# Optimization experiments

Hardware: AMD Instinct MI355X
Metric: run time of the kernel (lower is better)

Reference implementation:

```python
import jax, jax.numpy as jnp
import numpy as np

B, N, H_IN, H_HID, N_HEAD = 32, 500, 64, 16, 8
N_VALID = 400  # valid (non-padded) nodes per graph; node 0 is the root
NEG_INF = -1e20


def setup_inputs() -> dict:
    key = jax.random.key(0)
    ks = jax.random.split(key, 10)
    x = jax.random.normal(ks[0], (B, N, H_IN), jnp.float32)
    # sparse-ish binary adjacency with self loops
    A = (jax.random.uniform(ks[1], (B, N, N)) < 0.05).astype(jnp.float32)
    A = jnp.maximum(A, jnp.eye(N, dtype=jnp.float32)[None])
    # mask_nonzero: first N_VALID nodes of every graph are valid
    mask_batch = jnp.repeat(jnp.arange(B, dtype=jnp.int32), N_VALID)
    mask_row = jnp.tile(jnp.arange(N_VALID, dtype=jnp.int32), B)
    s = 0.1
    w1 = jax.random.normal(ks[2], (N_HEAD, H_IN, H_HID), jnp.float32) * s
    a_src1 = jax.random.normal(ks[3], (N_HEAD, H_HID), jnp.float32) * s
    a_dst1 = jax.random.normal(ks[4], (N_HEAD, H_HID), jnp.float32) * s
    w2 = jax.random.normal(ks[5], (1, N_HEAD * H_HID, H_IN), jnp.float32) * s
    a_src2 = jax.random.normal(ks[6], (1, H_IN), jnp.float32) * s
    a_dst2 = jax.random.normal(ks[7], (1, H_IN), jnp.float32) * s
    attn_w = jax.random.normal(ks[8], (2 * H_IN,), jnp.float32) * s
    return {"x": x, "A": A, "mask_batch": mask_batch, "mask_row": mask_row,
            "w1": w1, "a_src1": a_src1, "a_dst1": a_dst1,
            "w2": w2, "a_src2": a_src2, "a_dst2": a_dst2, "attn_w": attn_w}


def gat_layer(h_in, A, w, a_src, a_dst):
    # h_in: [B,N,F_in]; w: [H,F_in,F_out]
    h = jnp.einsum('bnf,hfo->bhno', h_in, w)              # [B,H,N,F_out]
    e_src = jnp.einsum('bhno,ho->bhn', h, a_src)          # [B,H,N]
    e_dst = jnp.einsum('bhno,ho->bhn', h, a_dst)
    e = jax.nn.leaky_relu(e_src[..., :, None] + e_dst[..., None, :], 0.2)  # [B,H,N,N]
    e = jnp.where(A[:, None, :, :] > 0, e, NEG_INF)
    attn = jax.nn.softmax(e, axis=-1)
    return jnp.einsum('bhnm,bhmo->bhno', attn, h)         # [B,H,N,F_out]


def reference(x, A, mask_batch, mask_row, w1, a_src1, a_dst1, w2, a_src2, a_dst2, attn_w):
    b, n, _ = x.shape
    # BatchGAT encoder: layer 1 (multi-head, concat + ELU), layer 2 (1 head -> h_in)
    h1 = gat_layer(x, A, w1, a_src1, a_dst1)                       # [B,H,N,h_hid]
    h1 = jax.nn.elu(h1).transpose(0, 2, 1, 3).reshape(b, n, -1)    # [B,N,H*h_hid]
    xc = gat_layer(h1, A, w2, a_src2, a_dst2)[:, 0]                # [B,N,h_in]
    # zero out padded nodes (so their Post_Attn scores are exactly 0)
    valid = jnp.zeros((b, n), x.dtype).at[mask_batch, mask_row].set(1.0)
    xc = xc * valid[:, :, None]
    # Post_Attn: scatter root features to each valid node position
    root = jnp.zeros_like(xc).at[mask_batch, mask_row, :].set(xc[mask_batch, 0, :])
    x_plus = jnp.concatenate([xc, root], axis=-1)                  # [B,N,2*h_in]
    score = x_plus @ attn_w                                        # [B,N]
    score = jnp.where(score == 0, NEG_INF, score)[:, :, None]      # masked_fill
    attn = jax.nn.softmax(score, axis=1)                           # softmax over nodes
    pooled = jnp.einsum('bnf,bn->bf', xc, attn[:, :, 0])           # [B,h_in]
    return pooled, attn
```

## Files before the change

### kernel.cpp

```cpp
#include <hip/hip_runtime.h>

#define NB 32
#define NN 500
#define HIN 64
#define HHID 16
#define NHEAD 8
#define NVALID 400
#define MAXK 128
#define NEG_INF -1e20f

__global__ __launch_bounds__(256) void k_pre(const float* __restrict__ A,
                                             int* __restrict__ nbr, int* __restrict__ cnt,
                                             const float* __restrict__ x, const float* __restrict__ w1,
                                             const float* __restrict__ as1, const float* __restrict__ ad1,
                                             float* __restrict__ h1p, float* __restrict__ e1s,
                                             float* __restrict__ e1d)
{
    int bid = blockIdx.x;
    if (bid < 4000) {
        int row = bid * 4 + (threadIdx.x >> 6);
        int lane = threadIdx.x & 63;
        const float4* arow4 = (const float4*)(A + (size_t)row * NN);
        int* np = nbr + (size_t)row * MAXK;
        int c = 0;
#pragma unroll
        for (int it = 0; it < 2; ++it) {
            int idx = it * 64 + lane;
            float4 av;
            if (idx < 125) av = arow4[idx];
            else { av.x = av.y = av.z = av.w = 0.f; }
            bool v0 = av.x > 0.f, v1 = av.y > 0.f, v2 = av.z > 0.f, v3 = av.w > 0.f;
            unsigned long long b0 = __ballot(v0), b1 = __ballot(v1);
            unsigned long long b2 = __ballot(v2), b3 = __ballot(v3);
            unsigned long long below = (1ull << lane) - 1ull;
            int p = c + __popcll(b0 & below) + __popcll(b1 & below)
                      + __popcll(b2 & below) + __popcll(b3 & below);
            int col = idx * 4;
            if (v0 && p < MAXK) np[p] = col;     p += (int)v0;
            if (v1 && p < MAXK) np[p] = col + 1; p += (int)v1;
            if (v2 && p < MAXK) np[p] = col + 2; p += (int)v2;
            if (v3 && p < MAXK) np[p] = col + 3; p += (int)v3;
            c += (int)(__popcll(b0) + __popcll(b1) + __popcll(b2) + __popcll(b3));
        }
        if (lane == 0) cnt[row] = c < MAXK ? c : MAXK;
        return;
    }
    int pb = bid - 4000;
    int b = pb >> 5, chunk = pb & 31;
    int t = threadIdx.x, slot = t >> 7, lane = t & 127;
    int h = lane >> 4, o = lane & 15;
    float wreg[64];
#pragma unroll
    for (int f = 0; f < 64; ++f) wreg[f] = w1[h * 1024 + f * 16 + o];
    float as_r = as1[h * 16 + o], ad_r = ad1[h * 16 + o];
    __shared__ __align__(16) float xs[16][64];
    {
        int node = chunk * 16 + (t >> 4);
        float4 v = make_float4(0.f, 0.f, 0.f, 0.f);
        if (node < NN) v = *(const float4*)&x[(size_t)(b * NN + node) * HIN + ((t * 4) & 63)];
        *(float4*)&xs[t >> 4][(t * 4) & 63] = v;
    }
    __syncthreads();
    for (int i = 0; i < 8; ++i) {
        int n = chunk * 16 + i * 2 + slot;
        if (n < NN) {
            const float* xrow = xs[i * 2 + slot];
            float acc = 0.f;
#pragma unroll
            for (int f4 = 0; f4 < 16; ++f4) {
                float4 xv = *(const float4*)&xrow[f4 * 4];
                acc += xv.x * wreg[f4 * 4] + xv.y * wreg[f4 * 4 + 1]
                     + xv.z * wreg[f4 * 4 + 2] + xv.w * wreg[f4 * 4 + 3];
            }
            h1p[(size_t)(b * NN + n) * 128 + lane] = acc;
            float vs = acc * as_r, vd = acc * ad_r;
#pragma unroll
            for (int m = 1; m < 16; m <<= 1) { vs += __shfl_xor(vs, m); vd += __shfl_xor(vd, m); }
            if (o == 0) {
                e1s[(size_t)(b * NN + n) * 8 + h] = vs;
                e1d[(size_t)(b * NN + n) * 8 + h] = vd;
            }
        }
    }
}

__global__ __launch_bounds__(128) void k_agg1p2(const int* __restrict__ nbr, const int* __restrict__ cnt,
                                                const float* __restrict__ h1p, const float* __restrict__ e1s,
                                                const float* __restrict__ e1d, const float* __restrict__ w2,
                                                const float* __restrict__ as2, const float* __restrict__ ad2,
                                                float* __restrict__ h2p, float* __restrict__ e2s,
                                                float* __restrict__ e2d)
{
    int bid = blockIdx.x;
    int xcd = bid & 7, g = bid >> 3;
    int b = (g / NN) * 8 + xcd;
    int n = g % NN;
    int row = b * NN + n;
    int t = threadIdx.x;
    int h = t >> 4, o = t & 15;
    int half = t >> 6, o2 = t & 63;
    __shared__ int nb_s[MAXK];
    __shared__ float p_s[NHEAD][MAXK + 4];
    __shared__ __align__(16) float hc[128];
    __shared__ float part[128];
    int K = cnt[row];
    for (int k = t; k < K; k += 128) nb_s[k] = nbr[(size_t)row * MAXK + k];
    __syncthreads();
    float es = e1s[(size_t)row * 8 + h];
    float r[8];
    float mx = -1e30f;
#pragma unroll
    for (int j = 0; j < 8; ++j) {
        int k = o + j * 16;
        if (k < K) {
            float e = es + e1d[(size_t)(b * NN + nb_s[k]) * 8 + h];
            e = e > 0.f ? e : 0.2f * e;
            r[j] = e;
            mx = fmaxf(mx, e);
        }
    }
#pragma unroll
    for (int m = 1; m < 16; m <<= 1) mx = fmaxf(mx, __shfl_xor(mx, m));
    float sum = 0.f;
#pragma unroll
    for (int j = 0; j < 8; ++j) {
        int k = o + j * 16;
        if (k < K) { float v = __expf(r[j] - mx); r[j] = v; sum += v; }
    }
#pragma unroll
    for (int m = 1; m < 16; m <<= 1) sum += __shfl_xor(sum, m);
    float inv = 1.f / sum;
#pragma unroll
    for (int j = 0; j < 8; ++j) {
        int k = o + j * 16;
        if (k < K) p_s[h][k] = r[j] * inv;
    }
    __syncthreads();
    float acc = 0.f;
    const float* hp = h1p + (size_t)b * NN * 128 + t;
    int k = 0;
    for (; k + 8 <= K; k += 8) {
        float a0 = hp[(size_t)nb_s[k] * 128];
        float a1 = hp[(size_t)nb_s[k + 1] * 128];
        float a2 = hp[(size_t)nb_s[k + 2] * 128];
        float a3 = hp[(size_t)nb_s[k + 3] * 128];
        float a4 = hp[(size_t)nb_s[k + 4] * 128];
        float a5 = hp[(size_t)nb_s[k + 5] * 128];
        float a6 = hp[(size_t)nb_s[k + 6] * 128];
        float a7 = hp[(size_t)nb_s[k + 7] * 128];
        acc += p_s[h][k] * a0;
        acc += p_s[h][k + 1] * a1;
        acc += p_s[h][k + 2] * a2;
        acc += p_s[h][k + 3] * a3;
        acc += p_s[h][k + 4] * a4;
        acc += p_s[h][k + 5] * a5;
        acc += p_s[h][k + 6] * a6;
        acc += p_s[h][k + 7] * a7;
    }
    for (; k < K; ++k) acc += p_s[h][k] * hp[(size_t)nb_s[k] * 128];
    hc[t] = acc > 0.f ? acc : expm1f(acc);
    __syncthreads();
    const float* wbase = w2 + (size_t)(half * 64) * 64 + o2;
    float acc2 = 0.f;
#pragma unroll
    for (int j4 = 0; j4 < 16; ++j4) {
        float4 hv = *(const float4*)&hc[half * 64 + j4 * 4];
        acc2 += hv.x * wbase[(j4 * 4 + 0) * 64] + hv.y * wbase[(j4 * 4 + 1) * 64]
              + hv.z * wbase[(j4 * 4 + 2) * 64] + hv.w * wbase[(j4 * 4 + 3) * 64];
    }
    part[t] = acc2;
    __syncthreads();
    if (half == 0) {
        float val = acc2 + part[64 + o2];
        h2p[(size_t)row * 64 + o2] = val;
        float vs = val * as2[o2], vd = val * ad2[o2];
#pragma unroll
        for (int m = 1; m < 64; m <<= 1) { vs += __shfl_xor(vs, m); vd += __shfl_xor(vd, m); }
        if (o2 == 0) { e2s[row] = vs; e2d[row] = vd; }
    }
}

__global__ __launch_bounds__(64) void k_agg2(const int* __restrict__ nbr, const int* __restrict__ cnt,
                                             const float* __restrict__ h2p, const float* __restrict__ e2s,
                                             const float* __restrict__ e2d, const float* __restrict__ aw,
                                             float* __restrict__ xc, float* __restrict__ sc,
                                             float* __restrict__ root_dot)
{
    int bid = blockIdx.x;
    int xcd = bid & 7, g = bid >> 3;
    int b = (g / NN) * 8 + xcd;
    int n = g % NN;
    int row = b * NN + n;
    int t = threadIdx.x;
    if (n >= NVALID) { xc[(size_t)row * 64 + t] = 0.f; return; }
    __shared__ int nb_s[MAXK];
    __shared__ float p_s[MAXK];
    int K = cnt[row];
    int nb0 = 0, nb1 = 0;
    if (t < K)      { nb0 = nbr[(size_t)row * MAXK + t];      nb_s[t] = nb0; }
    if (t + 64 < K) { nb1 = nbr[(size_t)row * MAXK + t + 64]; nb_s[t + 64] = nb1; }
    __syncthreads();
    float es = e2s[row];
    float r0 = -1e30f, r1 = -1e30f;
    if (t < K) {
        float e = es + e2d[b * NN + nb0];
        r0 = e > 0.f ? e : 0.2f * e;
    }
    if (t + 64 < K) {
        float e = es + e2d[b * NN + nb1];
        r1 = e > 0.f ? e : 0.2f * e;
    }
    float mx = fmaxf(r0, r1);
#pragma unroll
    for (int m = 1; m < 64; m <<= 1) mx = fmaxf(mx, __shfl_xor(mx, m));
    float v0 = (t < K) ? __expf(r0 - mx) : 0.f;
    float v1 = (t + 64 < K) ? __expf(r1 - mx) : 0.f;
    float sum = v0 + v1;
#pragma unroll
    for (int m = 1; m < 64; m <<= 1) sum += __shfl_xor(sum, m);
    float inv = 1.f / sum;
    if (t < K) p_s[t] = v0 * inv;
    if (t + 64 < K) p_s[t + 64] = v1 * inv;
    __syncthreads();
    float acc = 0.f;
    const float* h2b = h2p + (size_t)b * NN * 64 + t;
    int k = 0;
    for (; k + 8 <= K; k += 8) {
        float a0 = h2b[(size_t)nb_s[k] * 64];
        float a1 = h2b[(size_t)nb_s[k + 1] * 64];
        float a2 = h2b[(size_t)nb_s[k + 2] * 64];
        float a3 = h2b[(size_t)nb_s[k + 3] * 64];
        float a4 = h2b[(size_t)nb_s[k + 4] * 64];
        float a5 = h2b[(size_t)nb_s[k + 5] * 64];
        float a6 = h2b[(size_t)nb_s[k + 6] * 64];
        float a7 = h2b[(size_t)nb_s[k + 7] * 64];
        acc += p_s[k] * a0;
        acc += p_s[k + 1] * a1;
        acc += p_s[k + 2] * a2;
        acc += p_s[k + 3] * a3;
        acc += p_s[k + 4] * a4;
        acc += p_s[k + 5] * a5;
        acc += p_s[k + 6] * a6;
        acc += p_s[k + 7] * a7;
    }
    for (; k < K; ++k) acc += p_s[k] * h2b[(size_t)nb_s[k] * 64];
    xc[(size_t)row * 64 + t] = acc;
    float v = acc * aw[t];
#pragma unroll
    for (int m = 1; m < 64; m <<= 1) v += __shfl_xor(v, m);
    if (t == 0) sc[row] = v;
    if (n == 0) {
        float v2 = acc * aw[64 + t];
#pragma unroll
        for (int m = 1; m < 64; m <<= 1) v2 += __shfl_xor(v2, m);
        if (t == 0) root_dot[b] = v2;
    }
}

__global__ __launch_bounds__(1024) void k_pool(const float* __restrict__ xc, const float* __restrict__ sc,
                                               const float* __restrict__ root_dot, float* __restrict__ out)
{
    int b = blockIdx.x;
    int t = threadIdx.x, w = t >> 6, lane = t & 63;
    __shared__ float attn_s[NN];
    __shared__ float red[16];
    __shared__ float part[16][64];
    const float* xb = xc + (size_t)b * NN * 64;
    float rd = root_dot[b];
    float s = NEG_INF;
    if (t < NVALID) {
        s = sc[b * NN + t] + rd;
        if (s == 0.f) s = NEG_INF;
    }
    float mx = s;
#pragma unroll
    for (int m = 1; m < 64; m <<= 1) mx = fmaxf(mx, __shfl_xor(mx, m));
    if (lane == 0) red[w] = mx;
    __syncthreads();
    mx = red[0];
#pragma unroll
    for (int i = 1; i < 16; ++i) mx = fmaxf(mx, red[i]);
    float e = (t < NN) ? __expf(s - mx) : 0.f;
    float sum = e;
#pragma unroll
    for (int m = 1; m < 64; m <<= 1) sum += __shfl_xor(sum, m);
    __syncthreads();
    if (lane == 0) red[w] = sum;
    __syncthreads();
    sum = 0.f;
#pragma unroll
    for (int i = 0; i < 16; ++i) sum += red[i];
    float inv = 1.f / sum;
    if (t < NN) {
        float a = e * inv;
        out[NB * 64 + b * NN + t] = a;
        attn_s[t] = a;
    }
    __syncthreads();
    float acc = 0.f;
    for (int n = w; n < NN; n += 16) acc += attn_s[n] * xb[(size_t)n * 64 + lane];
    part[w][lane] = acc;
    __syncthreads();
    if (t < 64) {
        float v = 0.f;
#pragma unroll
        for (int i = 0; i < 16; ++i) v += part[i][t];
        out[b * 64 + t] = v;
    }
}

extern "C" void kernel_launch(void* const* d_in, const int* in_sizes, int n_in,
                              void* d_out, int out_size, void* d_ws, size_t ws_size,
                              hipStream_t stream) {
    const float* x   = (const float*)d_in[0];
    const float* A   = (const float*)d_in[1];
    const float* w1  = (const float*)d_in[4];
    const float* as1 = (const float*)d_in[5];
    const float* ad1 = (const float*)d_in[6];
    const float* w2  = (const float*)d_in[7];
    const float* as2 = (const float*)d_in[8];
    const float* ad2 = (const float*)d_in[9];
    const float* aw  = (const float*)d_in[10];
    float* out = (float*)d_out;

    char* ws = (char*)d_ws;
    int* nbr = (int*)ws;
    int* cnt = (int*)(ws + (size_t)16000 * 128 * 4);
    float* f = (float*)(ws + (size_t)16000 * 129 * 4);
    float* h1p   = f;  f += (size_t)NB * NN * 128;
    float* e1s   = f;  f += (size_t)NB * NN * NHEAD;
    float* e1d   = f;  f += (size_t)NB * NN * NHEAD;
    float* h2p   = f;  f += (size_t)NB * NN * 64;
    float* e2s   = f;  f += (size_t)NB * NN;
    float* e2d   = f;  f += (size_t)NB * NN;
    float* xc    = f;  f += (size_t)NB * NN * 64;
    float* sc    = f;  f += (size_t)NB * NN;
    float* rootd = f;  f += NB;

    hipLaunchKernelGGL(k_pre,    dim3(5024),    dim3(256), 0, stream, A, nbr, cnt, x, w1, as1, ad1, h1p, e1s, e1d);
    hipLaunchKernelGGL(k_agg1p2, dim3(NB * NN), dim3(128), 0, stream, nbr, cnt, h1p, e1s, e1d, w2, as2, ad2, h2p, e2s, e2d);
    hipLaunchKernelGGL(k_agg2,   dim3(NB * NN), dim3(64),  0, stream, nbr, cnt, h2p, e2s, e2d, aw, xc, sc, rootd);
    hipLaunchKernelGGL(k_pool,   dim3(NB),      dim3(1024), 0, stream, xc, sc, rootd, out);
}
```

Before: 159.8 us.

## Fuse second-layer aggregation into pooling kernel and reorder k_pre block roles

```diff
diff --git a/kernel.cpp b/kernel.cpp
--- a/kernel.cpp
+++ b/kernel.cpp
@@ -17,8 +17,8 @@
                                              float* __restrict__ e1d)
 {
     int bid = blockIdx.x;
-    if (bid < 4000) {
-        int row = bid * 4 + (threadIdx.x >> 6);
+    if (bid >= 1024) {
+        int row = (bid - 1024) * 4 + (threadIdx.x >> 6);
         int lane = threadIdx.x & 63;
         const float4* arow4 = (const float4*)(A + (size_t)row * NN);
         int* np = nbr + (size_t)row * MAXK;
@@ -45,7 +45,7 @@
         if (lane == 0) cnt[row] = c < MAXK ? c : MAXK;
         return;
     }
-    int pb = bid - 4000;
+    int pb = bid;
     int b = pb >> 5, chunk = pb & 31;
     int t = threadIdx.x, slot = t >> 7, lane = t & 127;
     int h = lane >> 4, o = lane & 15;
@@ -180,96 +180,88 @@
     }
 }
 
-__global__ __launch_bounds__(64) void k_agg2(const int* __restrict__ nbr, const int* __restrict__ cnt,
-                                             const float* __restrict__ h2p, const float* __restrict__ e2s,
-                                             const float* __restrict__ e2d, const float* __restrict__ aw,
-                                             float* __restrict__ xc, float* __restrict__ sc,
-                                             float* __restrict__ root_dot)
-{
-    int bid = blockIdx.x;
-    int xcd = bid & 7, g = bid >> 3;
-    int b = (g / NN) * 8 + xcd;
-    int n = g % NN;
-    int row = b * NN + n;
-    int t = threadIdx.x;
-    if (n >= NVALID) { xc[(size_t)row * 64 + t] = 0.f; return; }
-    __shared__ int nb_s[MAXK];
-    __shared__ float p_s[MAXK];
-    int K = cnt[row];
-    int nb0 = 0, nb1 = 0;
-    if (t < K)      { nb0 = nbr[(size_t)row * MAXK + t];      nb_s[t] = nb0; }
-    if (t + 64 < K) { nb1 = nbr[(size_t)row * MAXK + t + 64]; nb_s[t + 64] = nb1; }
-    __syncthreads();
-    float es = e2s[row];
-    float r0 = -1e30f, r1 = -1e30f;
-    if (t < K) {
-        float e = es + e2d[b * NN + nb0];
-        r0 = e > 0.f ? e : 0.2f * e;
-    }
-    if (t + 64 < K) {
-        float e = es + e2d[b * NN + nb1];
-        r1 = e > 0.f ? e : 0.2f * e;
-    }
-    float mx = fmaxf(r0, r1);
-#pragma unroll
-    for (int m = 1; m < 64; m <<= 1) mx = fmaxf(mx, __shfl_xor(mx, m));
-    float v0 = (t < K) ? __expf(r0 - mx) : 0.f;
-    float v1 = (t + 64 < K) ? __expf(r1 - mx) : 0.f;
-    float sum = v0 + v1;
-#pragma unroll
-    for (int m = 1; m < 64; m <<= 1) sum += __shfl_xor(sum, m);
-    float inv = 1.f / sum;
-    if (t < K) p_s[t] = v0 * inv;
-    if (t + 64 < K) p_s[t + 64] = v1 * inv;
-    __syncthreads();
-    float acc = 0.f;
-    const float* h2b = h2p + (size_t)b * NN * 64 + t;
-    int k = 0;
-    for (; k + 8 <= K; k += 8) {
-        float a0 = h2b[(size_t)nb_s[k] * 64];
-        float a1 = h2b[(size_t)nb_s[k + 1] * 64];
-        float a2 = h2b[(size_t)nb_s[k + 2] * 64];
-        float a3 = h2b[(size_t)nb_s[k + 3] * 64];
-        float a4 = h2b[(size_t)nb_s[k + 4] * 64];
-        float a5 = h2b[(size_t)nb_s[k + 5] * 64];
-        float a6 = h2b[(size_t)nb_s[k + 6] * 64];
-        float a7 = h2b[(size_t)nb_s[k + 7] * 64];
-        acc += p_s[k] * a0;
-        acc += p_s[k + 1] * a1;
-        acc += p_s[k + 2] * a2;
-        acc += p_s[k + 3] * a3;
-        acc += p_s[k + 4] * a4;
-        acc += p_s[k + 5] * a5;
-        acc += p_s[k + 6] * a6;
-        acc += p_s[k + 7] * a7;
-    }
-    for (; k < K; ++k) acc += p_s[k] * h2b[(size_t)nb_s[k] * 64];
-    xc[(size_t)row * 64 + t] = acc;
-    float v = acc * aw[t];
-#pragma unroll
-    for (int m = 1; m < 64; m <<= 1) v += __shfl_xor(v, m);
-    if (t == 0) sc[row] = v;
-    if (n == 0) {
-        float v2 = acc * aw[64 + t];
-#pragma unroll
-        for (int m = 1; m < 64; m <<= 1) v2 += __shfl_xor(v2, m);
-        if (t == 0) root_dot[b] = v2;
-    }
-}
-
-__global__ __launch_bounds__(1024) void k_pool(const float* __restrict__ xc, const float* __restrict__ sc,
-                                               const float* __restrict__ root_dot, float* __restrict__ out)
+__global__ __launch_bounds__(1024) void k_a2pool(const int* __restrict__ nbr, const int* __restrict__ cnt,
+                                                 const float* __restrict__ h2p, const float* __restrict__ e2s,
+                                                 const float* __restrict__ e2d, const float* __restrict__ aw,
+                                                 float* __restrict__ xc, float* __restrict__ out)
 {
     int b = blockIdx.x;
     int t = threadIdx.x, w = t >> 6, lane = t & 63;
+    __shared__ int nb_s[16][MAXK];
+    __shared__ float p_s[16][MAXK];
+    __shared__ float sc_s[NVALID];
+    __shared__ float rd_s;
     __shared__ float attn_s[NN];
     __shared__ float red[16];
     __shared__ float part[16][64];
-    const float* xb = xc + (size_t)b * NN * 64;
-    float rd = root_dot[b];
+    float aw0 = aw[lane], aw1 = aw[64 + lane];
+    const float* h2b = h2p + (size_t)b * NN * 64 + lane;
+    for (int n = w; n < NN; n += 16) {
+        int row = b * NN + n;
+        if (n >= NVALID) { xc[(size_t)row * 64 + lane] = 0.f; continue; }
+        int K = cnt[row];
+        int nb0 = 0, nb1 = 0;
+        if (lane < K)      { nb0 = nbr[(size_t)row * MAXK + lane];      nb_s[w][lane] = nb0; }
+        if (lane + 64 < K) { nb1 = nbr[(size_t)row * MAXK + lane + 64]; nb_s[w][lane + 64] = nb1; }
+        float es = e2s[row];
+        float r0 = -1e30f, r1 = -1e30f;
+        if (lane < K) {
+            float e = es + e2d[b * NN + nb0];
+            r0 = e > 0.f ? e : 0.2f * e;
+        }
+        if (lane + 64 < K) {
+            float e = es + e2d[b * NN + nb1];
+            r1 = e > 0.f ? e : 0.2f * e;
+        }
+        float mx = fmaxf(r0, r1);
+#pragma unroll
+        for (int m = 1; m < 64; m <<= 1) mx = fmaxf(mx, __shfl_xor(mx, m));
+        float v0 = (lane < K) ? __expf(r0 - mx) : 0.f;
+        float v1 = (lane + 64 < K) ? __expf(r1 - mx) : 0.f;
+        float sum = v0 + v1;
+#pragma unroll
+        for (int m = 1; m < 64; m <<= 1) sum += __shfl_xor(sum, m);
+        float inv = 1.f / sum;
+        if (lane < K) p_s[w][lane] = v0 * inv;
+        if (lane + 64 < K) p_s[w][lane + 64] = v1 * inv;
+        float acc = 0.f;
+        int k = 0;
+        for (; k + 8 <= K; k += 8) {
+            float a0 = h2b[(size_t)nb_s[w][k] * 64];
+            float a1 = h2b[(size_t)nb_s[w][k + 1] * 64];
+            float a2 = h2b[(size_t)nb_s[w][k + 2] * 64];
+            float a3 = h2b[(size_t)nb_s[w][k + 3] * 64];
+            float a4 = h2b[(size_t)nb_s[w][k + 4] * 64];
+            float a5 = h2b[(size_t)nb_s[w][k + 5] * 64];
+            float a6 = h2b[(size_t)nb_s[w][k + 6] * 64];
+            float a7 = h2b[(size_t)nb_s[w][k + 7] * 64];
+            acc += p_s[w][k] * a0;
+            acc += p_s[w][k + 1] * a1;
+            acc += p_s[w][k + 2] * a2;
+            acc += p_s[w][k + 3] * a3;
+            acc += p_s[w][k + 4] * a4;
+            acc += p_s[w][k + 5] * a5;
+            acc += p_s[w][k + 6] * a6;
+            acc += p_s[w][k + 7] * a7;
+        }
+        for (; k < K; ++k) acc += p_s[w][k] * h2b[(size_t)nb_s[w][k] * 64];
+        xc[(size_t)row * 64 + lane] = acc;
+        float v = acc * aw0;
+#pragma unroll
+        for (int m = 1; m < 64; m <<= 1) v += __shfl_xor(v, m);
+        if (lane == 0) sc_s[n] = v;
+        if (n == 0) {
+            float v2 = acc * aw1;
+#pragma unroll
+            for (int m = 1; m < 64; m <<= 1) v2 += __shfl_xor(v2, m);
+            if (lane == 0) rd_s = v2;
+        }
+    }
+    __syncthreads();
+    float rd = rd_s;
     float s = NEG_INF;
     if (t < NVALID) {
-        s = sc[b * NN + t] + rd;
+        s = sc_s[t] + rd;
         if (s == 0.f) s = NEG_INF;
     }
     float mx = s;
@@ -297,6 +289,7 @@
         attn_s[t] = a;
     }
     __syncthreads();
+    const float* xb = xc + (size_t)b * NN * 64;
     float acc = 0.f;
     for (int n = w; n < NN; n += 16) acc += attn_s[n] * xb[(size_t)n * 64 + lane];
     part[w][lane] = acc;
@@ -334,11 +327,8 @@
     float* e2s   = f;  f += (size_t)NB * NN;
     float* e2d   = f;  f += (size_t)NB * NN;
     float* xc    = f;  f += (size_t)NB * NN * 64;
-    float* sc    = f;  f += (size_t)NB * NN;
-    float* rootd = f;  f += NB;
-
-    hipLaunchKernelGGL(k_pre,    dim3(5024),    dim3(256), 0, stream, A, nbr, cnt, x, w1, as1, ad1, h1p, e1s, e1d);
-    hipLaunchKernelGGL(k_agg1p2, dim3(NB * NN), dim3(128), 0, stream, nbr, cnt, h1p, e1s, e1d, w2, as2, ad2, h2p, e2s, e2d);
-    hipLaunchKernelGGL(k_agg2,   dim3(NB * NN), dim3(64),  0, stream, nbr, cnt, h2p, e2s, e2d, aw, xc, sc, rootd);
-    hipLaunchKernelGGL(k_pool,   dim3(NB),      dim3(1024), 0, stream, xc, sc, rootd, out);
+
+    hipLaunchKernelGGL(k_pre,    dim3(5024),    dim3(256),  0, stream, A, nbr, cnt, x, w1, as1, ad1, h1p, e1s, e1d);
+    hipLaunchKernelGGL(k_agg1p2, dim3(NB * NN), dim3(128),  0, stream, nbr, cnt, h1p, e1s, e1d, w2, as2, ad2, h2p, e2s, e2d);
+    hipLaunchKernelGGL(k_a2pool, dim3(NB),      dim3(1024), 0, stream, nbr, cnt, h2p, e2s, e2d, aw, xc, out);
 }
```

Result: slower. 214.9 us (+34.5%).
